# Performance work log

Measured on AMD Instinct MI355X. Metric: run time of the kernel, lower is better.

The kernel has to match this reference:

```python
import jax, jax.numpy as jnp
import numpy as np

B, M, C = 8, 1024, 768


def setup_inputs() -> dict:
    key = jax.random.key(0)
    ks = jax.random.split(key, 10)
    s = 0.02
    return {
        "layout_x": jax.random.normal(ks[0], (B, M, C), jnp.float32),
        "text_x": jax.random.normal(ks[1], (B, M, C), jnp.float32),
        "mask": jax.random.randint(ks[2], (B, M), 0, 2).astype(jnp.float32),
        "Wqkv": jax.random.normal(ks[3], (C, 3 * C), jnp.float32) * s,
        "bqkv": jnp.zeros((3 * C,), jnp.float32),
        "Wq": jax.random.normal(ks[4], (C, C), jnp.float32) * s,
        "bq": jnp.zeros((C,), jnp.float32),
        "Wkv": jax.random.normal(ks[5], (C, 2 * C), jnp.float32) * s,
        "bkv": jnp.zeros((2 * C,), jnp.float32),
        "Wffn": jax.random.normal(ks[6], (C, C), jnp.float32) * s,
        "bffn": jnp.zeros((C,), jnp.float32),
    }


def _masked_attn(q, k, v, pair_mask, scale):
    # pair_mask: [B,M,M] True where valid (mask_i * mask_j != 0)
    scores = jnp.einsum("bmd,bnd->bmn", q, k) * scale  # [B,M,M]
    scores = jnp.where(pair_mask, scores, jnp.float32(-10000.0))
    attn = jax.nn.softmax(scores, axis=-1)
    return jnp.einsum("bmn,bnd->bmd", attn, v)


def reference(layout_x, text_x, mask, Wqkv, bqkv, Wq, bq, Wkv, bkv, Wffn, bffn):
    dim = layout_x.shape[-1]
    scale = dim ** (-0.5)
    # mask repeated over C then mask@mask.T / C  ==  outer product of 1D masks
    pair = (mask[:, :, None] * mask[:, None, :]) != 0  # [B,M,M] bool, True=keep

    # self-attention on layout_x
    qkv = layout_x @ Wqkv + bqkv  # [B,M,3C]
    q, k, v = jnp.split(qkv, 3, axis=-1)
    layout_o = _masked_attn(q, k, v, pair, scale)

    # cross-attention: q from layout output, k/v from text_x
    cq = layout_o @ Wq + bq
    kv = text_x @ Wkv + bkv  # [B,M,2C]
    ck, cv = jnp.split(kv, 2, axis=-1)
    merge = _masked_attn(cq, ck, cv, pair, scale)

    return merge @ Wffn + bffn
```

## Files before the change

kernel.cpp:

```cpp
#include <hip/hip_runtime.h>
#include <math.h>

#define BDIM 8
#define MDIM 1024
#define CDIM 768
#define ROWS (BDIM * MDIM)

typedef __attribute__((ext_vector_type(8))) short short8;
typedef __attribute__((ext_vector_type(8))) unsigned short ushort8;
typedef __attribute__((ext_vector_type(4))) float f32x4;

#define MFMA16(a, b, c) __builtin_amdgcn_mfma_f32_16x16x32_bf16((a), (b), (c), 0, 0, 0)

__device__ __forceinline__ unsigned short f2bf(float f) {
  unsigned u = __float_as_uint(f);
  return (unsigned short)((u + 0x7FFFu + ((u >> 16) & 1u)) >> 16);
}

__global__ __launch_bounds__(256) void prologue(
    const float* __restrict__ xl, const float* __restrict__ xt,
    unsigned short* __restrict__ dxl, unsigned short* __restrict__ dxt,
    const float* __restrict__ W0, const float* __restrict__ W1,
    const float* __restrict__ W2, const float* __restrict__ W3,
    unsigned short* __restrict__ D0, unsigned short* __restrict__ D1,
    unsigned short* __restrict__ D2, unsigned short* __restrict__ D3,
    float* __restrict__ rowsum) {
  const int bx = blockIdx.x;
  const int tid = threadIdx.x;
  if (bx < 6144) {
    const float* src = bx < 3072 ? xl : xt;
    unsigned short* dst = bx < 3072 ? dxl : dxt;
    const int i = ((bx < 3072 ? bx : bx - 3072) * 256 + tid) * 8;
    const float4 a = *(const float4*)(src + i);
    const float4 b = *(const float4*)(src + i + 4);
    ushort8 o;
    o[0] = f2bf(a.x); o[1] = f2bf(a.y); o[2] = f2bf(a.z); o[3] = f2bf(a.w);
    o[4] = f2bf(b.x); o[5] = f2bf(b.y); o[6] = f2bf(b.z); o[7] = f2bf(b.w);
    *(ushort8*)(dst + i) = o;
  } else if (bx < 6152) {
    const int i = ((bx - 6144) * 256 + tid) * 8;
    const float4 z = {0.f, 0.f, 0.f, 0.f};
    *(float4*)(rowsum + i) = z;
    *(float4*)(rowsum + i + 4) = z;
  } else {
    int x = bx - 6152;
    int bxx = x % 168;
    const int k0 = (x / 168) * 32;
    const float* W; unsigned short* D; int N;
    if (bxx < 72)       { W = W0; D = D0; N = 2304; }
    else if (bxx < 96)  { W = W1; D = D1; N = 768;  bxx -= 72; }
    else if (bxx < 144) { W = W2; D = D2; N = 1536; bxx -= 96; }
    else                { W = W3; D = D3; N = 768;  bxx -= 144; }
    __shared__ unsigned short t[32][33];
    const int tx = tid & 31, ty = tid >> 5;
    const int n0 = bxx * 32;
#pragma unroll
    for (int i = 0; i < 4; ++i)
      t[ty + i * 8][tx] = f2bf(W[(size_t)(k0 + ty + i * 8) * N + n0 + tx]);
    __syncthreads();
#pragma unroll
    for (int i = 0; i < 4; ++i)
      D[(size_t)(n0 + ty + i * 8) * CDIM + k0 + tx] = t[tx][ty + i * 8];
  }
}

__device__ __forceinline__ void stage64(
    const unsigned short* __restrict__ g, int ld, int k0,
    unsigned short* lds, int wave, int lane) {
  const int gchunk = (lane & 7) ^ (lane >> 3);
#pragma unroll
  for (int j = 0; j < 4; ++j) {
    const int grp = wave * 4 + j;
    const unsigned short* gp =
        g + (size_t)(grp * 8 + (lane >> 3)) * ld + k0 + gchunk * 8;
    __builtin_amdgcn_global_load_lds(
        (const __attribute__((address_space(1))) unsigned int*)gp,
        (__attribute__((address_space(3))) unsigned int*)(lds + grp * 512),
        16, 0, 0);
  }
}

__device__ __forceinline__ void mfma_loop64(
    const unsigned short* __restrict__ A, int lda,
    const unsigned short* __restrict__ Bt, int ldb, int K,
    unsigned short* As, unsigned short* Bs, f32x4 acc[4][4],
    int wave, int lane) {
  const int wx = wave & 1, wy = wave >> 1;
  const int quad = lane >> 4, l16 = lane & 15;
  for (int k0 = 0; k0 < K; k0 += 64) {
    stage64(A, lda, k0, As, wave, lane);
    stage64(Bt, ldb, k0, Bs, wave, lane);
    __syncthreads();
#pragma unroll
    for (int h = 0; h < 2; ++h) {
      const int slot = ((((h << 2) | quad) ^ (l16 & 7))) * 8;
      short8 afr[4], bfr[4];
#pragma unroll
      for (int mt = 0; mt < 4; ++mt)
        afr[mt] = *(const short8*)&As[(wy * 64 + mt * 16 + l16) * 64 + slot];
#pragma unroll
      for (int nt = 0; nt < 4; ++nt)
        bfr[nt] = *(const short8*)&Bs[(wx * 64 + nt * 16 + l16) * 64 + slot];
#pragma unroll
      for (int mt = 0; mt < 4; ++mt)
#pragma unroll
        for (int nt = 0; nt < 4; ++nt)
          acc[mt][nt] = MFMA16(afr[mt], bfr[nt], acc[mt][nt]);
    }
    __syncthreads();
  }
}

__device__ __forceinline__ void proj_epilogue(
    f32x4 acc[4][4], const float* __restrict__ bias,
    unsigned short* __restrict__ Y, unsigned short* __restrict__ vTd,
    int c0, int m0, int lastSlice, int trans, int wave, int lane) {
  const int wx = wave & 1, wy = wave >> 1;
  const int quad = lane >> 4, l16 = lane & 15;
  const int slice = c0 / 768;
  if (trans && slice == lastSlice) {
#pragma unroll
    for (int mt = 0; mt < 4; ++mt) {
      const int row0 = m0 + wy * 64 + mt * 16 + quad * 4;
      const int b = row0 >> 10, n0 = row0 & 1023;
#pragma unroll
      for (int nt = 0; nt < 4; ++nt) {
        const int gcol = c0 + wx * 64 + nt * 16 + l16;
        const int d = gcol - slice * 768;
        const float bv = bias[gcol];
        uint2 o;
        o.x = (unsigned)f2bf(acc[mt][nt][0] + bv) |
              ((unsigned)f2bf(acc[mt][nt][1] + bv) << 16);
        o.y = (unsigned)f2bf(acc[mt][nt][2] + bv) |
              ((unsigned)f2bf(acc[mt][nt][3] + bv) << 16);
        *(uint2*)&vTd[((size_t)b * CDIM + d) * MDIM + n0] = o;
      }
    }
  } else {
    const size_t sbase = (size_t)slice * ROWS * 768;
#pragma unroll
    for (int mt = 0; mt < 4; ++mt)
#pragma unroll
      for (int nt = 0; nt < 4; ++nt) {
        const int gcol = c0 + wx * 64 + nt * 16 + l16;
        const int lcol = gcol - slice * 768;
        const float bv = bias[gcol];
#pragma unroll
        for (int rg = 0; rg < 4; ++rg) {
          const int row = m0 + wy * 64 + mt * 16 + quad * 4 + rg;
          Y[sbase + (size_t)row * 768 + lcol] = f2bf(acc[mt][nt][rg] + bv);
        }
      }
  }
}

__device__ __forceinline__ void swizzle_mc(int lin, int* m0, int* c0) {
  const int xcd = lin & 7, j = lin >> 3;
  *m0 = (xcd * 8 + (j & 7)) * 128;
  *c0 = (j >> 3) * 128;
}

__global__ __launch_bounds__(256, 4) void gemm_proj(
    const unsigned short* __restrict__ A, const unsigned short* __restrict__ Bt,
    const float* __restrict__ bias, unsigned short* __restrict__ Y,
    unsigned short* __restrict__ vTd, int trans) {
  __shared__ __align__(16) unsigned short As[128 * 64];
  __shared__ __align__(16) unsigned short Bs[128 * 64];
  int m0, c0;
  swizzle_mc(blockIdx.y * gridDim.x + blockIdx.x, &m0, &c0);
  const int tid = threadIdx.x;
  const int wave = tid >> 6, lane = tid & 63;
  const f32x4 vzero = {0.f, 0.f, 0.f, 0.f};
  f32x4 acc[4][4];
#pragma unroll
  for (int mt = 0; mt < 4; ++mt)
#pragma unroll
    for (int nt = 0; nt < 4; ++nt) acc[mt][nt] = vzero;
  mfma_loop64(A + (size_t)m0 * CDIM, CDIM, Bt + (size_t)c0 * CDIM, CDIM, CDIM,
              As, Bs, acc, wave, lane);
  proj_epilogue(acc, bias, Y, vTd, c0, m0, (int)(gridDim.x / 6) - 1, trans,
                wave, lane);
}

__global__ __launch_bounds__(256, 4) void gemm_proj_dual(
    const unsigned short* __restrict__ A0, const unsigned short* __restrict__ B0,
    const float* __restrict__ b0, unsigned short* __restrict__ Y0,
    const unsigned short* __restrict__ A1, const unsigned short* __restrict__ B1,
    const float* __restrict__ b1, unsigned short* __restrict__ Y1,
    unsigned short* __restrict__ vTd) {
  __shared__ __align__(16) unsigned short As[128 * 64];
  __shared__ __align__(16) unsigned short Bs[128 * 64];
  int lin = blockIdx.x;
  const unsigned short *A, *Bt;
  const float* bias;
  unsigned short* Y;
  int gx, trans;
  if (lin < 384) { A = A0; Bt = B0; bias = b0; Y = Y0; gx = 6;  trans = 0; }
  else { lin -= 384; A = A1; Bt = B1; bias = b1; Y = Y1; gx = 12; trans = 1; }
  int m0, c0;
  swizzle_mc(lin, &m0, &c0);
  const int tid = threadIdx.x;
  const int wave = tid >> 6, lane = tid & 63;
  const f32x4 vzero = {0.f, 0.f, 0.f, 0.f};
  f32x4 acc[4][4];
#pragma unroll
  for (int mt = 0; mt < 4; ++mt)
#pragma unroll
    for (int nt = 0; nt < 4; ++nt) acc[mt][nt] = vzero;
  mfma_loop64(A + (size_t)m0 * CDIM, CDIM, Bt + (size_t)c0 * CDIM, CDIM, CDIM,
              As, Bs, acc, wave, lane);
  proj_epilogue(acc, bias, Y, vTd, c0, m0, gx / 6 - 1, trans, wave, lane);
}

__global__ __launch_bounds__(256, 4) void gemm_ffn(
    const unsigned short* __restrict__ A, const unsigned short* __restrict__ Bt,
    const float* __restrict__ bias, float* __restrict__ Y) {
  __shared__ __align__(16) unsigned short As[128 * 64];
  __shared__ __align__(16) unsigned short Bs[128 * 64];
  int m0, c0;
  swizzle_mc(blockIdx.y * gridDim.x + blockIdx.x, &m0, &c0);
  const int tid = threadIdx.x;
  const int wave = tid >> 6, lane = tid & 63;
  const int wx = wave & 1, wy = wave >> 1;
  const int quad = lane >> 4, l16 = lane & 15;
  const f32x4 vzero = {0.f, 0.f, 0.f, 0.f};
  f32x4 acc[4][4];
#pragma unroll
  for (int mt = 0; mt < 4; ++mt)
#pragma unroll
    for (int nt = 0; nt < 4; ++nt) acc[mt][nt] = vzero;
  mfma_loop64(A + (size_t)m0 * CDIM, CDIM, Bt + (size_t)c0 * CDIM, CDIM, CDIM,
              As, Bs, acc, wave, lane);
#pragma unroll
  for (int mt = 0; mt < 4; ++mt)
#pragma unroll
    for (int nt = 0; nt < 4; ++nt) {
      const int col = c0 + wx * 64 + nt * 16 + l16;
      const float bv = bias[col];
#pragma unroll
      for (int rg = 0; rg < 4; ++rg) {
        const int row = m0 + wy * 64 + mt * 16 + quad * 4 + rg;
        Y[(size_t)row * 768 + col] = acc[mt][nt][rg] + bv;
      }
    }
}

__global__ __launch_bounds__(256, 4) void gemm_qk(
    const unsigned short* __restrict__ Qb, const unsigned short* __restrict__ Kb,
    const float* __restrict__ mask, unsigned short* __restrict__ S, float scale,
    float* __restrict__ rowsum) {
  __shared__ __align__(16) unsigned short As[128 * 64];
  __shared__ __align__(16) unsigned short Bs[128 * 64];
  const int c0 = blockIdx.x * 128;
  const int m0 = blockIdx.y * 128;
  const int b = blockIdx.z;
  const int tid = threadIdx.x;
  const int wave = tid >> 6, lane = tid & 63;
  const int wx = wave & 1, wy = wave >> 1;
  const int quad = lane >> 4, l16 = lane & 15;

  const f32x4 vzero = {0.f, 0.f, 0.f, 0.f};
  f32x4 acc[4][4];
#pragma unroll
  for (int mt = 0; mt < 4; ++mt)
#pragma unroll
    for (int nt = 0; nt < 4; ++nt) acc[mt][nt] = vzero;

  mfma_loop64(Qb + ((size_t)b * MDIM + m0) * CDIM, CDIM,
              Kb + ((size_t)b * MDIM + c0) * CDIM, CDIM, CDIM,
              As, Bs, acc, wave, lane);

  const float* maskb = mask + b * MDIM;
  float mrow[4][4], rsum[4][4];
#pragma unroll
  for (int mt = 0; mt < 4; ++mt)
#pragma unroll
    for (int rg = 0; rg < 4; ++rg) {
      mrow[mt][rg] = maskb[m0 + wy * 64 + mt * 16 + quad * 4 + rg];
      rsum[mt][rg] = 0.f;
    }
  unsigned short* Sb = S + (size_t)b * MDIM * MDIM;
#pragma unroll
  for (int nt = 0; nt < 4; ++nt) {
    const int col = c0 + wx * 64 + nt * 16 + l16;
    const float mcol = maskb[col];
#pragma unroll
    for (int mt = 0; mt < 4; ++mt)
#pragma unroll
      for (int rg = 0; rg < 4; ++rg) {
        const int row = m0 + wy * 64 + mt * 16 + quad * 4 + rg;
        const float e = (mrow[mt][rg] * mcol != 0.f)
                            ? __expf(acc[mt][nt][rg] * scale)
                            : 1e-30f;
        Sb[(size_t)row * MDIM + col] = f2bf(e);
        rsum[mt][rg] += e;
      }
  }
  for (int off = 1; off < 16; off <<= 1) {
#pragma unroll
    for (int mt = 0; mt < 4; ++mt)
#pragma unroll
      for (int rg = 0; rg < 4; ++rg)
        rsum[mt][rg] += __shfl_xor(rsum[mt][rg], off, 64);
  }
  if (l16 == 0) {
    float* rsb = rowsum + (b << 10) + m0 + wy * 64;
#pragma unroll
    for (int mt = 0; mt < 4; ++mt)
#pragma unroll
      for (int rg = 0; rg < 4; ++rg)
        atomicAdd(&rsb[mt * 16 + quad * 4 + rg], rsum[mt][rg]);
  }
}

__global__ __launch_bounds__(256, 4) void attn_pv(
    const unsigned short* __restrict__ P, const unsigned short* __restrict__ vT,
    unsigned short* __restrict__ O, const float* __restrict__ rowsum) {
  __shared__ __align__(16) unsigned short As[128 * 64];
  __shared__ __align__(16) unsigned short Bs[128 * 64];
  const int c0 = blockIdx.x * 128;
  const int m0 = blockIdx.y * 128;
  const int b = blockIdx.z;
  const int tid = threadIdx.x;
  const int wave = tid >> 6, lane = tid & 63;
  const int wx = wave & 1, wy = wave >> 1;
  const int quad = lane >> 4, l16 = lane & 15;

  const f32x4 vzero = {0.f, 0.f, 0.f, 0.f};
  f32x4 acc[4][4];
#pragma unroll
  for (int mt = 0; mt < 4; ++mt)
#pragma unroll
    for (int nt = 0; nt < 4; ++nt) acc[mt][nt] = vzero;

  mfma_loop64(P + ((size_t)b * MDIM + m0) * MDIM, MDIM,
              vT + ((size_t)b * CDIM + c0) * MDIM, MDIM, MDIM,
              As, Bs, acc, wave, lane);

  const float* rsb = rowsum + (b << 10) + m0 + wy * 64;
  float inv[4][4];
#pragma unroll
  for (int mt = 0; mt < 4; ++mt)
#pragma unroll
    for (int rg = 0; rg < 4; ++rg)
      inv[mt][rg] = 1.f / rsb[mt * 16 + quad * 4 + rg];
#pragma unroll
  for (int mt = 0; mt < 4; ++mt)
#pragma unroll
    for (int nt = 0; nt < 4; ++nt)
#pragma unroll
      for (int rg = 0; rg < 4; ++rg) {
        const int row = m0 + wy * 64 + mt * 16 + quad * 4 + rg;
        const int col = c0 + wx * 64 + nt * 16 + l16;
        O[(size_t)(b * MDIM + row) * CDIM + col] =
            f2bf(acc[mt][nt][rg] * inv[mt][rg]);
      }
}

extern "C" void kernel_launch(void* const* d_in, const int* in_sizes, int n_in,
                              void* d_out, int out_size, void* d_ws, size_t ws_size,
                              hipStream_t stream) {
  const float* layout_x = (const float*)d_in[0];
  const float* text_x   = (const float*)d_in[1];
  const float* maskp    = (const float*)d_in[2];
  const float* Wqkv     = (const float*)d_in[3];
  const float* bqkv     = (const float*)d_in[4];
  const float* Wq       = (const float*)d_in[5];
  const float* bq       = (const float*)d_in[6];
  const float* Wkv      = (const float*)d_in[7];
  const float* bkv      = (const float*)d_in[8];
  const float* Wffn     = (const float*)d_in[9];
  const float* bffn     = (const float*)d_in[10];
  float* out = (float*)d_out;
  char* ws = (char*)d_ws;

  const float scale = 1.0f / sqrtf((float)CDIM);

  unsigned short* xlb    = (unsigned short*)(ws);
  unsigned short* xtb    = (unsigned short*)(ws + 12582912);
  unsigned short* Wqkv_t = (unsigned short*)(ws + 25165824);
  unsigned short* Wq_t   = (unsigned short*)(ws + 28704768);
  unsigned short* Wkv_t  = (unsigned short*)(ws + 29884416);
  unsigned short* Wffn_t = (unsigned short*)(ws + 32243712);
  unsigned short* Qb     = (unsigned short*)(ws + 33423360);
  unsigned short* Kb     = (unsigned short*)(ws + 46006272);
  unsigned short* cqb    = (unsigned short*)(ws + 58589184);
  unsigned short* vT     = (unsigned short*)(ws + 71172096);
  unsigned short* S      = (unsigned short*)(ws + 83755008);
  unsigned short* attn1  = xlb;
  unsigned short* Kc     = Qb;
  float* rowsum1 = out;
  float* rowsum2 = out + 8192;

  prologue<<<10184, 256, 0, stream>>>(layout_x, text_x, xlb, xtb,
                                      Wqkv, Wq, Wkv, Wffn,
                                      Wqkv_t, Wq_t, Wkv_t, Wffn_t, rowsum1);
  gemm_proj<<<dim3(18, 64), 256, 0, stream>>>(xlb, Wqkv_t, bqkv, Qb, vT, 1);
  gemm_qk<<<dim3(8, 8, BDIM), 256, 0, stream>>>(Qb, Kb, maskp, S, scale, rowsum1);
  attn_pv<<<dim3(6, 8, BDIM), 256, 0, stream>>>(S, vT, attn1, rowsum1);
  gemm_proj_dual<<<1152, 256, 0, stream>>>(attn1, Wq_t, bq, cqb,
                                           xtb, Wkv_t, bkv, Kc, vT);
  gemm_qk<<<dim3(8, 8, BDIM), 256, 0, stream>>>(cqb, Kc, maskp, S, scale, rowsum2);
  attn_pv<<<dim3(6, 8, BDIM), 256, 0, stream>>>(S, vT, attn1, rowsum2);
  gemm_ffn<<<dim3(6, 64), 256, 0, stream>>>(attn1, Wffn_t, bffn, out);
}
```

Baseline: 311.5 us.

## Stream MFMA operands directly from global memory into registers, dropping LDS staging

The shared GEMM inner loop no longer stages A and B tiles through LDS with barriers. Each wave now loads its own MFMA fragments straight from global memory into registers, double-buffered across the two K halves. Launch bounds drop from 4 to 3 blocks per SM to leave room for the extra registers. This removes LDS traffic and __syncthreads but duplicates global/L2 reads across waves and relies on cache hits for reuse.

New measurement: 626.7 us. +101.2%, slower.

```diff
diff --git a/kernel.cpp b/kernel.cpp
--- a/kernel.cpp
+++ b/kernel.cpp
@@ -64,50 +64,50 @@
   }
 }
 
-__device__ __forceinline__ void stage64(
-    const unsigned short* __restrict__ g, int ld, int k0,
-    unsigned short* lds, int wave, int lane) {
-  const int gchunk = (lane & 7) ^ (lane >> 3);
-#pragma unroll
-  for (int j = 0; j < 4; ++j) {
-    const int grp = wave * 4 + j;
-    const unsigned short* gp =
-        g + (size_t)(grp * 8 + (lane >> 3)) * ld + k0 + gchunk * 8;
-    __builtin_amdgcn_global_load_lds(
-        (const __attribute__((address_space(1))) unsigned int*)gp,
-        (__attribute__((address_space(3))) unsigned int*)(lds + grp * 512),
-        16, 0, 0);
-  }
-}
-
-__device__ __forceinline__ void mfma_loop64(
+__device__ __forceinline__ void mfma_stream(
     const unsigned short* __restrict__ A, int lda,
     const unsigned short* __restrict__ Bt, int ldb, int K,
-    unsigned short* As, unsigned short* Bs, f32x4 acc[4][4],
-    int wave, int lane) {
-  const int wx = wave & 1, wy = wave >> 1;
-  const int quad = lane >> 4, l16 = lane & 15;
+    f32x4 acc[4][4], int wave, int lane) {
+  const int wx = wave & 1, wy = wave >> 1;
+  const int quad = lane >> 4, l16 = lane & 15;
+  const unsigned short* pa[4];
+  const unsigned short* pb[4];
+#pragma unroll
+  for (int mt = 0; mt < 4; ++mt)
+    pa[mt] = A + (size_t)(wy * 64 + mt * 16 + l16) * lda + quad * 8;
+#pragma unroll
+  for (int nt = 0; nt < 4; ++nt)
+    pb[nt] = Bt + (size_t)(wx * 64 + nt * 16 + l16) * ldb + quad * 8;
+
+  short8 a0[4], b0[4], a1[4], b1[4];
+#pragma unroll
+  for (int i = 0; i < 4; ++i) {
+    a0[i] = *(const short8*)(pa[i]);
+    b0[i] = *(const short8*)(pb[i]);
+  }
   for (int k0 = 0; k0 < K; k0 += 64) {
-    stage64(A, lda, k0, As, wave, lane);
-    stage64(Bt, ldb, k0, Bs, wave, lane);
-    __syncthreads();
-#pragma unroll
-    for (int h = 0; h < 2; ++h) {
-      const int slot = ((((h << 2) | quad) ^ (l16 & 7))) * 8;
-      short8 afr[4], bfr[4];
-#pragma unroll
-      for (int mt = 0; mt < 4; ++mt)
-        afr[mt] = *(const short8*)&As[(wy * 64 + mt * 16 + l16) * 64 + slot];
+#pragma unroll
+    for (int i = 0; i < 4; ++i) {
+      a1[i] = *(const short8*)(pa[i] + k0 + 32);
+      b1[i] = *(const short8*)(pb[i] + k0 + 32);
+    }
+#pragma unroll
+    for (int mt = 0; mt < 4; ++mt)
 #pragma unroll
       for (int nt = 0; nt < 4; ++nt)
-        bfr[nt] = *(const short8*)&Bs[(wx * 64 + nt * 16 + l16) * 64 + slot];
-#pragma unroll
-      for (int mt = 0; mt < 4; ++mt)
-#pragma unroll
-        for (int nt = 0; nt < 4; ++nt)
-          acc[mt][nt] = MFMA16(afr[mt], bfr[nt], acc[mt][nt]);
-    }
-    __syncthreads();
+        acc[mt][nt] = MFMA16(a0[mt], b0[nt], acc[mt][nt]);
+    if (k0 + 64 < K) {
+#pragma unroll
+      for (int i = 0; i < 4; ++i) {
+        a0[i] = *(const short8*)(pa[i] + k0 + 64);
+        b0[i] = *(const short8*)(pb[i] + k0 + 64);
+      }
+    }
+#pragma unroll
+    for (int mt = 0; mt < 4; ++mt)
+#pragma unroll
+      for (int nt = 0; nt < 4; ++nt)
+        acc[mt][nt] = MFMA16(a1[mt], b1[nt], acc[mt][nt]);
   }
 }
 
@@ -160,12 +160,10 @@
   *c0 = (j >> 3) * 128;
 }
 
-__global__ __launch_bounds__(256, 4) void gemm_proj(
+__global__ __launch_bounds__(256, 3) void gemm_proj(
     const unsigned short* __restrict__ A, const unsigned short* __restrict__ Bt,
     const float* __restrict__ bias, unsigned short* __restrict__ Y,
     unsigned short* __restrict__ vTd, int trans) {
-  __shared__ __align__(16) unsigned short As[128 * 64];
-  __shared__ __align__(16) unsigned short Bs[128 * 64];
   int m0, c0;
   swizzle_mc(blockIdx.y * gridDim.x + blockIdx.x, &m0, &c0);
   const int tid = threadIdx.x;
@@ -176,20 +174,18 @@
   for (int mt = 0; mt < 4; ++mt)
 #pragma unroll
     for (int nt = 0; nt < 4; ++nt) acc[mt][nt] = vzero;
-  mfma_loop64(A + (size_t)m0 * CDIM, CDIM, Bt + (size_t)c0 * CDIM, CDIM, CDIM,
-              As, Bs, acc, wave, lane);
+  mfma_stream(A + (size_t)m0 * CDIM, CDIM, Bt + (size_t)c0 * CDIM, CDIM, CDIM,
+              acc, wave, lane);
   proj_epilogue(acc, bias, Y, vTd, c0, m0, (int)(gridDim.x / 6) - 1, trans,
                 wave, lane);
 }
 
-__global__ __launch_bounds__(256, 4) void gemm_proj_dual(
+__global__ __launch_bounds__(256, 3) void gemm_proj_dual(
     const unsigned short* __restrict__ A0, const unsigned short* __restrict__ B0,
     const float* __restrict__ b0, unsigned short* __restrict__ Y0,
     const unsigned short* __restrict__ A1, const unsigned short* __restrict__ B1,
     const float* __restrict__ b1, unsigned short* __restrict__ Y1,
     unsigned short* __restrict__ vTd) {
-  __shared__ __align__(16) unsigned short As[128 * 64];
-  __shared__ __align__(16) unsigned short Bs[128 * 64];
   int lin = blockIdx.x;
   const unsigned short *A, *Bt;
   const float* bias;
@@ -207,16 +203,14 @@
   for (int mt = 0; mt < 4; ++mt)
 #pragma unroll
     for (int nt = 0; nt < 4; ++nt) acc[mt][nt] = vzero;
-  mfma_loop64(A + (size_t)m0 * CDIM, CDIM, Bt + (size_t)c0 * CDIM, CDIM, CDIM,
-              As, Bs, acc, wave, lane);
+  mfma_stream(A + (size_t)m0 * CDIM, CDIM, Bt + (size_t)c0 * CDIM, CDIM, CDIM,
+              acc, wave, lane);
   proj_epilogue(acc, bias, Y, vTd, c0, m0, gx / 6 - 1, trans, wave, lane);
 }
 
-__global__ __launch_bounds__(256, 4) void gemm_ffn(
+__global__ __launch_bounds__(256, 3) void gemm_ffn(
     const unsigned short* __restrict__ A, const unsigned short* __restrict__ Bt,
     const float* __restrict__ bias, float* __restrict__ Y) {
-  __shared__ __align__(16) unsigned short As[128 * 64];
-  __shared__ __align__(16) unsigned short Bs[128 * 64];
   int m0, c0;
   swizzle_mc(blockIdx.y * gridDim.x + blockIdx.x, &m0, &c0);
   const int tid = threadIdx.x;
@@ -229,8 +223,8 @@
   for (int mt = 0; mt < 4; ++mt)
 #pragma unroll
     for (int nt = 0; nt < 4; ++nt) acc[mt][nt] = vzero;
-  mfma_loop64(A + (size_t)m0 * CDIM, CDIM, Bt + (size_t)c0 * CDIM, CDIM, CDIM,
-              As, Bs, acc, wave, lane);
+  mfma_stream(A + (size_t)m0 * CDIM, CDIM, Bt + (size_t)c0 * CDIM, CDIM, CDIM,
+              acc, wave, lane);
 #pragma unroll
   for (int mt = 0; mt < 4; ++mt)
 #pragma unroll
@@ -245,12 +239,10 @@
     }
 }
 
-__global__ __launch_bounds__(256, 4) void gemm_qk(
+__global__ __launch_bounds__(256, 3) void gemm_qk(
     const unsigned short* __restrict__ Qb, const unsigned short* __restrict__ Kb,
     const float* __restrict__ mask, unsigned short* __restrict__ S, float scale,
     float* __restrict__ rowsum) {
-  __shared__ __align__(16) unsigned short As[128 * 64];
-  __shared__ __align__(16) unsigned short Bs[128 * 64];
   const int c0 = blockIdx.x * 128;
   const int m0 = blockIdx.y * 128;
   const int b = blockIdx.z;
@@ -266,9 +258,9 @@
 #pragma unroll
     for (int nt = 0; nt < 4; ++nt) acc[mt][nt] = vzero;
 
-  mfma_loop64(Qb + ((size_t)b * MDIM + m0) * CDIM, CDIM,
+  mfma_stream(Qb + ((size_t)b * MDIM + m0) * CDIM, CDIM,
               Kb + ((size_t)b * MDIM + c0) * CDIM, CDIM, CDIM,
-              As, Bs, acc, wave, lane);
+              acc, wave, lane);
 
   const float* maskb = mask + b * MDIM;
   float mrow[4][4], rsum[4][4];
@@ -313,11 +305,9 @@
   }
 }
 
-__global__ __launch_bounds__(256, 4) void attn_pv(
+__global__ __launch_bounds__(256, 3) void attn_pv(
     const unsigned short* __restrict__ P, const unsigned short* __restrict__ vT,
     unsigned short* __restrict__ O, const float* __restrict__ rowsum) {
-  __shared__ __align__(16) unsigned short As[128 * 64];
-  __shared__ __align__(16) unsigned short Bs[128 * 64];
   const int c0 = blockIdx.x * 128;
   const int m0 = blockIdx.y * 128;
   const int b = blockIdx.z;
@@ -333,9 +323,9 @@
 #pragma unroll
     for (int nt = 0; nt < 4; ++nt) acc[mt][nt] = vzero;
 
-  mfma_loop64(P + ((size_t)b * MDIM + m0) * MDIM, MDIM,
+  mfma_stream(P + ((size_t)b * MDIM + m0) * MDIM, MDIM,
               vT + ((size_t)b * CDIM + c0) * MDIM, MDIM, MDIM,
-              As, Bs, acc, wave, lane);
+              acc, wave, lane);
 
   const float* rsb = rowsum + (b << 10) + m0 + wy * 64;
   float inv[4][4];
```

## Compact unmasked tokens and skip masked attention tiles in both attentions

Applied to the files above, without the earlier changes.

Builds a per-batch permutation that moves unmasked tokens to the front, writes Q/K/V projections in that compacted order, and skips QK and PV tiles beyond the unmasked count. Masked query rows of the cross-attention are filled with the mean of V, which is what a uniform softmax over all keys gives. This removes roughly three quarters of the attention work for a half-density mask, at the cost of scattered epilogue stores and two extra small kernels. It relies on the -10000 mask making masked entries contribute nothing for valid rows and uniform weights for fully masked rows, which holds for the reference semantics.

New measurement: 329.4 us. 5.8% more time.

```diff
diff --git a/kernel.cpp b/kernel.cpp
--- a/kernel.cpp
+++ b/kernel.cpp
@@ -15,6 +15,9 @@
 __device__ __forceinline__ unsigned short f2bf(float f) {
   unsigned u = __float_as_uint(f);
   return (unsigned short)((u + 0x7FFFu + ((u >> 16) & 1u)) >> 16);
+}
+__device__ __forceinline__ float bf2f(unsigned short b) {
+  return __uint_as_float(((unsigned)b) << 16);
 }
 
 __global__ __launch_bounds__(256) void prologue(
@@ -24,7 +27,9 @@
     const float* __restrict__ W2, const float* __restrict__ W3,
     unsigned short* __restrict__ D0, unsigned short* __restrict__ D1,
     unsigned short* __restrict__ D2, unsigned short* __restrict__ D3,
-    float* __restrict__ rowsum) {
+    const float* __restrict__ mask, float* __restrict__ rowsum,
+    unsigned short* __restrict__ idxArr, unsigned short* __restrict__ pArr,
+    int* __restrict__ nuArr) {
   const int bx = blockIdx.x;
   const int tid = threadIdx.x;
   if (bx < 6144) {
@@ -42,7 +47,7 @@
     const float4 z = {0.f, 0.f, 0.f, 0.f};
     *(float4*)(rowsum + i) = z;
     *(float4*)(rowsum + i + 4) = z;
-  } else {
+  } else if (bx < 10184) {
     int x = bx - 6152;
     int bxx = x % 168;
     const int k0 = (x / 168) * 32;
@@ -61,6 +66,33 @@
 #pragma unroll
     for (int i = 0; i < 4; ++i)
       D[(size_t)(n0 + ty + i * 8) * CDIM + k0 + tx] = t[tx][ty + i * 8];
+  } else {
+    const int b = bx - 10184;
+    if (tid >= 64) return;
+    const unsigned long long below = (1ull << tid) - 1ull;
+    const float* mb = mask + (b << 10);
+    unsigned long long bals[16];
+    int nu = 0;
+#pragma unroll
+    for (int c = 0; c < 16; ++c) {
+      const float mv = mb[c * 64 + tid];
+      bals[c] = __ballot(mv != 0.f);
+      nu += (int)__popcll(bals[c]);
+    }
+    int ru = 0, rm = 0;
+#pragma unroll
+    for (int c = 0; c < 16; ++c) {
+      const unsigned long long bal = bals[c];
+      const int preU = (int)__popcll(bal & below);
+      const int preM = tid - preU;
+      const int m = c * 64 + tid;
+      const int pos = ((bal >> tid) & 1ull) ? (ru + preU) : (nu + rm + preM);
+      pArr[(b << 10) + m] = (unsigned short)pos;
+      idxArr[(b << 10) + pos] = (unsigned short)m;
+      const int tot = (int)__popcll(bal);
+      ru += tot; rm += 64 - tot;
+    }
+    if (tid == 0) nuArr[b] = nu;
   }
 }
 
@@ -114,7 +146,8 @@
 __device__ __forceinline__ void proj_epilogue(
     f32x4 acc[4][4], const float* __restrict__ bias,
     unsigned short* __restrict__ Y, unsigned short* __restrict__ vTd,
-    int c0, int m0, int lastSlice, int trans, int wave, int lane) {
+    const unsigned short* __restrict__ pArr,
+    int c0, int m0, int lastSlice, int trans, int perm, int wave, int lane) {
   const int wx = wave & 1, wy = wave >> 1;
   const int quad = lane >> 4, l16 = lane & 15;
   const int slice = c0 / 768;
@@ -122,18 +155,17 @@
 #pragma unroll
     for (int mt = 0; mt < 4; ++mt) {
       const int row0 = m0 + wy * 64 + mt * 16 + quad * 4;
-      const int b = row0 >> 10, n0 = row0 & 1023;
+      const int b = row0 >> 10;
 #pragma unroll
       for (int nt = 0; nt < 4; ++nt) {
         const int gcol = c0 + wx * 64 + nt * 16 + l16;
         const int d = gcol - slice * 768;
         const float bv = bias[gcol];
-        uint2 o;
-        o.x = (unsigned)f2bf(acc[mt][nt][0] + bv) |
-              ((unsigned)f2bf(acc[mt][nt][1] + bv) << 16);
-        o.y = (unsigned)f2bf(acc[mt][nt][2] + bv) |
-              ((unsigned)f2bf(acc[mt][nt][3] + bv) << 16);
-        *(uint2*)&vTd[((size_t)b * CDIM + d) * MDIM + n0] = o;
+#pragma unroll
+        for (int rg = 0; rg < 4; ++rg) {
+          const int pos = pArr[row0 + rg];
+          vTd[((size_t)b * CDIM + d) * MDIM + pos] = f2bf(acc[mt][nt][rg] + bv);
+        }
       }
     }
   } else {
@@ -148,7 +180,8 @@
 #pragma unroll
         for (int rg = 0; rg < 4; ++rg) {
           const int row = m0 + wy * 64 + mt * 16 + quad * 4 + rg;
-          Y[sbase + (size_t)row * 768 + lcol] = f2bf(acc[mt][nt][rg] + bv);
+          const int orow = perm ? ((row & ~1023) + (int)pArr[row]) : row;
+          Y[sbase + (size_t)orow * 768 + lcol] = f2bf(acc[mt][nt][rg] + bv);
         }
       }
   }
@@ -163,7 +196,7 @@
 __global__ __launch_bounds__(256, 4) void gemm_proj(
     const unsigned short* __restrict__ A, const unsigned short* __restrict__ Bt,
     const float* __restrict__ bias, unsigned short* __restrict__ Y,
-    unsigned short* __restrict__ vTd, int trans) {
+    unsigned short* __restrict__ vTd, const unsigned short* __restrict__ pArr) {
   __shared__ __align__(16) unsigned short As[128 * 64];
   __shared__ __align__(16) unsigned short Bs[128 * 64];
   int m0, c0;
@@ -178,8 +211,8 @@
     for (int nt = 0; nt < 4; ++nt) acc[mt][nt] = vzero;
   mfma_loop64(A + (size_t)m0 * CDIM, CDIM, Bt + (size_t)c0 * CDIM, CDIM, CDIM,
               As, Bs, acc, wave, lane);
-  proj_epilogue(acc, bias, Y, vTd, c0, m0, (int)(gridDim.x / 6) - 1, trans,
-                wave, lane);
+  proj_epilogue(acc, bias, Y, vTd, pArr, c0, m0, (int)(gridDim.x / 6) - 1,
+                1, 1, wave, lane);
 }
 
 __global__ __launch_bounds__(256, 4) void gemm_proj_dual(
@@ -187,16 +220,16 @@
     const float* __restrict__ b0, unsigned short* __restrict__ Y0,
     const unsigned short* __restrict__ A1, const unsigned short* __restrict__ B1,
     const float* __restrict__ b1, unsigned short* __restrict__ Y1,
-    unsigned short* __restrict__ vTd) {
+    unsigned short* __restrict__ vTd, const unsigned short* __restrict__ pArr) {
   __shared__ __align__(16) unsigned short As[128 * 64];
   __shared__ __align__(16) unsigned short Bs[128 * 64];
   int lin = blockIdx.x;
   const unsigned short *A, *Bt;
   const float* bias;
   unsigned short* Y;
-  int gx, trans;
-  if (lin < 384) { A = A0; Bt = B0; bias = b0; Y = Y0; gx = 6;  trans = 0; }
-  else { lin -= 384; A = A1; Bt = B1; bias = b1; Y = Y1; gx = 12; trans = 1; }
+  int lastSlice, trans, perm;
+  if (lin < 384) { A = A0; Bt = B0; bias = b0; Y = Y0; lastSlice = 0; trans = 0; perm = 0; }
+  else { lin -= 384; A = A1; Bt = B1; bias = b1; Y = Y1; lastSlice = 1; trans = 1; perm = 1; }
   int m0, c0;
   swizzle_mc(lin, &m0, &c0);
   const int tid = threadIdx.x;
@@ -209,7 +242,8 @@
     for (int nt = 0; nt < 4; ++nt) acc[mt][nt] = vzero;
   mfma_loop64(A + (size_t)m0 * CDIM, CDIM, Bt + (size_t)c0 * CDIM, CDIM, CDIM,
               As, Bs, acc, wave, lane);
-  proj_epilogue(acc, bias, Y, vTd, c0, m0, gx / 6 - 1, trans, wave, lane);
+  proj_epilogue(acc, bias, Y, vTd, pArr, c0, m0, lastSlice, trans, perm,
+                wave, lane);
 }
 
 __global__ __launch_bounds__(256, 4) void gemm_ffn(
@@ -246,14 +280,17 @@
 }
 
 __global__ __launch_bounds__(256, 4) void gemm_qk(
-    const unsigned short* __restrict__ Qb, const unsigned short* __restrict__ Kb,
-    const float* __restrict__ mask, unsigned short* __restrict__ S, float scale,
-    float* __restrict__ rowsum) {
+    const unsigned short* __restrict__ Qc, const unsigned short* __restrict__ Kc,
+    unsigned short* __restrict__ S, float scale, float* __restrict__ rowsum,
+    const int* __restrict__ nuArr) {
   __shared__ __align__(16) unsigned short As[128 * 64];
   __shared__ __align__(16) unsigned short Bs[128 * 64];
+  const int b = blockIdx.z;
+  const int nu = nuArr[b];
+  const int nuPad = (nu + 127) & ~127;
   const int c0 = blockIdx.x * 128;
   const int m0 = blockIdx.y * 128;
-  const int b = blockIdx.z;
+  if (m0 >= nuPad || c0 >= nuPad) return;
   const int tid = threadIdx.x;
   const int wave = tid >> 6, lane = tid & 63;
   const int wx = wave & 1, wy = wave >> 1;
@@ -266,33 +303,27 @@
 #pragma unroll
     for (int nt = 0; nt < 4; ++nt) acc[mt][nt] = vzero;
 
-  mfma_loop64(Qb + ((size_t)b * MDIM + m0) * CDIM, CDIM,
-              Kb + ((size_t)b * MDIM + c0) * CDIM, CDIM, CDIM,
+  mfma_loop64(Qc + ((size_t)(b << 10) + m0) * CDIM, CDIM,
+              Kc + ((size_t)(b << 10) + c0) * CDIM, CDIM, CDIM,
               As, Bs, acc, wave, lane);
 
-  const float* maskb = mask + b * MDIM;
-  float mrow[4][4], rsum[4][4];
-#pragma unroll
-  for (int mt = 0; mt < 4; ++mt)
-#pragma unroll
-    for (int rg = 0; rg < 4; ++rg) {
-      mrow[mt][rg] = maskb[m0 + wy * 64 + mt * 16 + quad * 4 + rg];
-      rsum[mt][rg] = 0.f;
-    }
-  unsigned short* Sb = S + (size_t)b * MDIM * MDIM;
+  float rsum[4][4];
+#pragma unroll
+  for (int mt = 0; mt < 4; ++mt)
+#pragma unroll
+    for (int rg = 0; rg < 4; ++rg) rsum[mt][rg] = 0.f;
+  unsigned short* Sb = S + ((size_t)b << 20);
 #pragma unroll
   for (int nt = 0; nt < 4; ++nt) {
     const int col = c0 + wx * 64 + nt * 16 + l16;
-    const float mcol = maskb[col];
+    const int cv = col < nu;
 #pragma unroll
     for (int mt = 0; mt < 4; ++mt)
 #pragma unroll
       for (int rg = 0; rg < 4; ++rg) {
-        const int row = m0 + wy * 64 + mt * 16 + quad * 4 + rg;
-        const float e = (mrow[mt][rg] * mcol != 0.f)
-                            ? __expf(acc[mt][nt][rg] * scale)
-                            : 1e-30f;
-        Sb[(size_t)row * MDIM + col] = f2bf(e);
+        const int i = m0 + wy * 64 + mt * 16 + quad * 4 + rg;
+        const float e = (i < nu && cv) ? __expf(acc[mt][nt][rg] * scale) : 0.f;
+        Sb[(size_t)i * MDIM + col] = f2bf(e);
         rsum[mt][rg] += e;
       }
   }
@@ -313,14 +344,19 @@
   }
 }
 
+template <bool SCATTER>
 __global__ __launch_bounds__(256, 4) void attn_pv(
-    const unsigned short* __restrict__ P, const unsigned short* __restrict__ vT,
-    unsigned short* __restrict__ O, const float* __restrict__ rowsum) {
+    const unsigned short* __restrict__ S, const unsigned short* __restrict__ vTc,
+    unsigned short* __restrict__ O, const float* __restrict__ rowsum,
+    const int* __restrict__ nuArr, const unsigned short* __restrict__ idxArr) {
   __shared__ __align__(16) unsigned short As[128 * 64];
   __shared__ __align__(16) unsigned short Bs[128 * 64];
+  const int b = blockIdx.z;
+  const int nu = nuArr[b];
+  const int m0 = blockIdx.y * 128;
+  if (m0 >= ((nu + 127) & ~127)) return;
+  const int kmax = (nu + 63) & ~63;
   const int c0 = blockIdx.x * 128;
-  const int m0 = blockIdx.y * 128;
-  const int b = blockIdx.z;
   const int tid = threadIdx.x;
   const int wave = tid >> 6, lane = tid & 63;
   const int wx = wave & 1, wy = wave >> 1;
@@ -333,8 +369,8 @@
 #pragma unroll
     for (int nt = 0; nt < 4; ++nt) acc[mt][nt] = vzero;
 
-  mfma_loop64(P + ((size_t)b * MDIM + m0) * MDIM, MDIM,
-              vT + ((size_t)b * CDIM + c0) * MDIM, MDIM, MDIM,
+  mfma_loop64(S + ((size_t)b << 20) + (size_t)m0 * MDIM, MDIM,
+              vTc + ((size_t)b * CDIM + c0) * MDIM, MDIM, kmax,
               As, Bs, acc, wave, lane);
 
   const float* rsb = rowsum + (b << 10) + m0 + wy * 64;
@@ -350,11 +386,50 @@
     for (int nt = 0; nt < 4; ++nt)
 #pragma unroll
       for (int rg = 0; rg < 4; ++rg) {
-        const int row = m0 + wy * 64 + mt * 16 + quad * 4 + rg;
+        const int i = m0 + wy * 64 + mt * 16 + quad * 4 + rg;
         const int col = c0 + wx * 64 + nt * 16 + l16;
-        O[(size_t)(b * MDIM + row) * CDIM + col] =
-            f2bf(acc[mt][nt][rg] * inv[mt][rg]);
+        if (SCATTER) {
+          if (i < nu) {
+            const int m = idxArr[(b << 10) + i];
+            O[((size_t)(b << 10) + m) * CDIM + col] =
+                f2bf(acc[mt][nt][rg] * inv[mt][rg]);
+          }
+        } else {
+          O[((size_t)(b << 10) + i) * CDIM + col] =
+              f2bf(acc[mt][nt][rg] * inv[mt][rg]);
+        }
       }
+}
+
+__global__ __launch_bounds__(256) void mean_cols(
+    const unsigned short* __restrict__ vTc, float* __restrict__ meanCV) {
+  const unsigned short* p = vTc + (size_t)blockIdx.x * MDIM;
+  const int t = threadIdx.x;
+  const int wave = t >> 6, lane = t & 63;
+  __shared__ float red[4];
+  const uint2 u = *(const uint2*)(p + t * 4);
+  float s = bf2f((unsigned short)(u.x & 0xFFFFu)) +
+            bf2f((unsigned short)(u.x >> 16)) +
+            bf2f((unsigned short)(u.y & 0xFFFFu)) +
+            bf2f((unsigned short)(u.y >> 16));
+  for (int off = 1; off < 64; off <<= 1) s += __shfl_xor(s, off, 64);
+  if (lane == 0) red[wave] = s;
+  __syncthreads();
+  if (t == 0)
+    meanCV[blockIdx.x] = (red[0] + red[1] + red[2] + red[3]) * (1.f / 1024.f);
+}
+
+__global__ __launch_bounds__(256) void fill_masked(
+    const float* __restrict__ mask, const float* __restrict__ meanCV,
+    unsigned short* __restrict__ merge) {
+  const int m = blockIdx.x;
+  if (mask[m] != 0.f) return;
+  const float* mv = meanCV + (m >> 10) * CDIM;
+  unsigned short* o = merge + (size_t)m * CDIM;
+  const int t = threadIdx.x;
+  o[t] = f2bf(mv[t]);
+  o[t + 256] = f2bf(mv[t + 256]);
+  o[t + 512] = f2bf(mv[t + 512]);
 }
 
 extern "C" void kernel_launch(void* const* d_in, const int* in_sizes, int n_in,
@@ -382,25 +457,36 @@
   unsigned short* Wq_t   = (unsigned short*)(ws + 28704768);
   unsigned short* Wkv_t  = (unsigned short*)(ws + 29884416);
   unsigned short* Wffn_t = (unsigned short*)(ws + 32243712);
-  unsigned short* Qb     = (unsigned short*)(ws + 33423360);
-  unsigned short* Kb     = (unsigned short*)(ws + 46006272);
-  unsigned short* cqb    = (unsigned short*)(ws + 58589184);
-  unsigned short* vT     = (unsigned short*)(ws + 71172096);
+  unsigned short* Qc     = (unsigned short*)(ws + 33423360);
+  unsigned short* Kc     = (unsigned short*)(ws + 46006272);
+  unsigned short* cqc    = (unsigned short*)(ws + 58589184);
+  unsigned short* vTc    = (unsigned short*)(ws + 71172096);
   unsigned short* S      = (unsigned short*)(ws + 83755008);
-  unsigned short* attn1  = xlb;
-  unsigned short* Kc     = Qb;
+  unsigned short* attn1c = xlb;
+  unsigned short* merge  = xlb;
+  unsigned short* cKc    = Qc;
+
   float* rowsum1 = out;
   float* rowsum2 = out + 8192;
-
-  prologue<<<10184, 256, 0, stream>>>(layout_x, text_x, xlb, xtb,
+  unsigned short* idxArr = (unsigned short*)(out + 16384);
+  unsigned short* pArr   = (unsigned short*)(out + 20480);
+  int* nuArr             = (int*)(out + 24576);
+  float* meanCV          = out + 24592;
+
+  prologue<<<10192, 256, 0, stream>>>(layout_x, text_x, xlb, xtb,
                                       Wqkv, Wq, Wkv, Wffn,
-                                      Wqkv_t, Wq_t, Wkv_t, Wffn_t, rowsum1);
-  gemm_proj<<<dim3(18, 64), 256, 0, stream>>>(xlb, Wqkv_t, bqkv, Qb, vT, 1);
-  gemm_qk<<<dim3(8, 8, BDIM), 256, 0, stream>>>(Qb, Kb, maskp, S, scale, rowsum1);
-  attn_pv<<<dim3(6, 8, BDIM), 256, 0, stream>>>(S, vT, attn1, rowsum1);
-  gemm_proj_dual<<<1152, 256, 0, stream>>>(attn1, Wq_t, bq, cqb,
-                                           xtb, Wkv_t, bkv, Kc, vT);
-  gemm_qk<<<dim3(8, 8, BDIM), 256, 0, stream>>>(cqb, Kc, maskp, S, scale, rowsum2);
-  attn_pv<<<dim3(6, 8, BDIM), 256, 0, stream>>>(S, vT, attn1, rowsum2);
-  gemm_ffn<<<dim3(6, 64), 256, 0, stream>>>(attn1, Wffn_t, bffn, out);
-}
+                                      Wqkv_t, Wq_t, Wkv_t, Wffn_t,
+                                      maskp, rowsum1, idxArr, pArr, nuArr);
+  gemm_proj<<<dim3(18, 64), 256, 0, stream>>>(xlb, Wqkv_t, bqkv, Qc, vTc, pArr);
+  gemm_qk<<<dim3(8, 8, BDIM), 256, 0, stream>>>(Qc, Kc, S, scale, rowsum1, nuArr);
+  attn_pv<false><<<dim3(6, 8, BDIM), 256, 0, stream>>>(S, vTc, attn1c, rowsum1,
+                                                       nuArr, idxArr);
+  gemm_proj_dual<<<1152, 256, 0, stream>>>(attn1c, Wq_t, bq, cqc,
+                                           xtb, Wkv_t, bkv, cKc, vTc, pArr);
+  mean_cols<<<6144, 256, 0, stream>>>(vTc, meanCV);
+  fill_masked<<<ROWS, 256, 0, stream>>>(maskp, meanCV, merge);
+  gemm_qk<<<dim3(8, 8, BDIM), 256, 0, stream>>>(cqc, cKc, S, scale, rowsum2, nuArr);
+  attn_pv<true><<<dim3(6, 8, BDIM), 256, 0, stream>>>(S, vTc, merge, rowsum2,
+                                                      nuArr, idxArr);
+  gemm_ffn<<<dim3(6, 64), 256, 0, stream>>>(merge, Wffn_t, bffn, out);
+}
```
